# Optimization experiments

Hardware: AMD Instinct MI355X
Metric: run time of the kernel (lower is better)

Reference implementation:

```python
import jax, jax.numpy as jnp
import numpy as np

BETA = 0.1
MARGIN = 0.1
LOSS_WEIGHT = 1.0
K = 4          # num_negative_samples_per_positive
EPS = 1e-6
C, D, P = 100000, 256, 65536


def _energy(p, c):
    """Euclidean entailment-cone energy: relu(apex_angle(p,c) - aperture(p))."""
    diff = c - p
    num = jnp.sum(c * c, -1) - jnp.sum(p * p, -1) - jnp.sum(diff * diff, -1)
    norm_p = jnp.linalg.norm(p, axis=-1)
    denom = 2.0 * norm_p * jnp.linalg.norm(diff, axis=-1) + EPS
    cosang = jnp.clip(num / denom, -1.0 + EPS, 1.0 - EPS)
    ang = jnp.arccos(cosang)
    aperture = jnp.arcsin(jnp.clip(BETA / (norm_p + EPS), 0.0, 1.0 - EPS))
    return jax.nn.relu(ang - aperture)


def setup_inputs() -> dict:
    key = jax.random.key(0)
    k1, k2, k3 = jax.random.split(key, 3)
    prototypes = jax.random.normal(k1, (C, D), dtype=jnp.float32)
    pairs = jax.random.randint(k2, (P, 2), 0, C, dtype=jnp.int32)
    neg_c = jax.random.randint(k3, (P * K,), 0, C, dtype=jnp.int32)
    return {"prototypes": prototypes, "pairs": pairs, "neg_c": neg_c}


def reference(prototypes, pairs, neg_c):
    # positive pairs: (parent, child) gathers
    p_pos = prototypes[pairs[:, 0]]                    # [P, D]
    c_pos = prototypes[pairs[:, 1]]                    # [P, D]
    avg_pos = _energy(p_pos, c_pos).mean()

    # negatives: each positive parent repeated K times vs sampled neg children
    neg_p_idx = jnp.repeat(pairs[:, 0], K)             # [P*K]
    p_neg = prototypes[neg_p_idx]                      # [P*K, D]
    c_neg = prototypes[neg_c]                          # [P*K, D]
    avg_neg = jax.nn.relu(MARGIN - _energy(p_neg, c_neg)).mean()

    return (avg_pos + avg_neg) * 0.5 * LOSS_WEIGHT
```

## Files before the change

kernel.cpp:

```cpp
#include <hip/hip_runtime.h>

#define BETA   0.1f
#define MARGIN 0.1f
#define EPSF   1e-6f
#define KNEG   4

typedef float f2_t __attribute__((ext_vector_type(2)));

__device__ __forceinline__ float gsum16(float v) {
    #pragma unroll
    for (int off = 8; off >= 1; off >>= 1) v += __shfl_xor(v, off, 64);
    return v;
}
__device__ __forceinline__ float wave_sum(float v) {
    #pragma unroll
    for (int off = 32; off >= 1; off >>= 1) v += __shfl_xor(v, off, 64);
    return v;
}
__device__ __forceinline__ float dot4(float4 a, float4 b) {
    return a.x*b.x + a.y*b.y + a.z*b.z + a.w*b.w;
}
__device__ __forceinline__ unsigned packf4(float4 v) {
    unsigned p = __builtin_amdgcn_cvt_pk_fp8_f32(v.x, v.y, 0u, false);
    return __builtin_amdgcn_cvt_pk_fp8_f32(v.z, v.w, p, true);
}
__device__ __forceinline__ void unpack4(unsigned u, float* f) {
    f2_t a = __builtin_amdgcn_cvt_pk_f32_fp8(u, false);
    f[0] = a.x; f[1] = a.y;
    a = __builtin_amdgcn_cvt_pk_f32_fp8(u, true);
    f[2] = a.x; f[3] = a.y;
}

__global__ __launch_bounds__(256) void cvt_fp8_norm(
    const float* __restrict__ in, uint4* __restrict__ tab,
    float* __restrict__ norm2, float* __restrict__ apert, int C)
{
    const int sl  = threadIdx.x & 15;
    const int row = (blockIdx.x * 256 + threadIdx.x) >> 4;
    if (row >= C) return;
    const float4* src = (const float4*)(in + (size_t)row * 256);
    float4 v0 = src[sl], v1 = src[sl + 16], v2 = src[sl + 32], v3 = src[sl + 48];
    uint4 u;
    u.x = packf4(v0); u.y = packf4(v1); u.z = packf4(v2); u.w = packf4(v3);
    tab[(size_t)row * 16 + sl] = u;
    float ss = gsum16(dot4(v0,v0) + dot4(v1,v1) + dot4(v2,v2) + dot4(v3,v3));
    if (sl == 0) {
        norm2[row] = ss;
        float np = sqrtf(ss);
        apert[row] = asinf(fminf(fmaxf(BETA / (np + EPSF), 0.f), 1.f - EPSF));
    }
}

__global__ __launch_bounds__(256) void cone_main_fp8(
    const uint4* __restrict__ tab,
    const float* __restrict__ norm2,
    const float* __restrict__ apert,
    const int*   __restrict__ pairs,
    const int*   __restrict__ negc,
    float*       __restrict__ part,
    int P)
{
    const int lane = threadIdx.x & 63;
    const int wid  = threadIdx.x >> 6;
    const int sub  = lane >> 4;
    const int sl   = lane & 15;
    const int pair = (blockIdx.x * 4 + wid) * 4 + sub;

    float pos_e = 0.f, neg_e = 0.f;
    if (pair < P) {
        const int pi = pairs[2 * pair];
        int idx[5];
        idx[0] = pairs[2 * pair + 1];
        #pragma unroll
        for (int k = 0; k < KNEG; ++k) idx[1 + k] = negc[4 * pair + k];

        uint4 pu = tab[(size_t)pi * 16 + sl];
        uint4 cu[5];
        #pragma unroll
        for (int j = 0; j < 5; ++j) cu[j] = tab[(size_t)idx[j] * 16 + sl];

        int tidx = (sl >= 2 && sl < 7) ? idx[sl - 2] : pi;
        const float* tbl = (sl == 1) ? apert : norm2;
        float sv = tbl[tidx];
        const int base = sub * 16;
        const float p2 = __shfl(sv, base + 0, 64);
        const float ap = __shfl(sv, base + 1, 64);
        const float np = sqrtf(p2);

        float pf[16];
        unpack4(pu.x, pf + 0);  unpack4(pu.y, pf + 4);
        unpack4(pu.z, pf + 8);  unpack4(pu.w, pf + 12);

        #pragma unroll
        for (int j = 0; j < 5; ++j) {
            float cf[16];
            unpack4(cu[j].x, cf + 0);  unpack4(cu[j].y, cf + 4);
            unpack4(cu[j].z, cf + 8);  unpack4(cu[j].w, cf + 12);
            float acc = 0.f;
            #pragma unroll
            for (int d = 0; d < 16; ++d) acc += cf[d] * pf[d];
            float dot = gsum16(acc);
            float c2  = __shfl(sv, base + 2 + j, 64);
            float num = 2.f * (dot - p2);
            float d2  = fmaxf(c2 + p2 - 2.f * dot, 0.f);
            float den = 2.f * np * sqrtf(d2) + EPSF;
            float ca  = fminf(fmaxf(num / den, -1.f + EPSF), 1.f - EPSF);
            float e   = fmaxf(acosf(ca) - ap, 0.f);
            if (j == 0) pos_e = e;
            else        neg_e += fmaxf(MARGIN - e, 0.f);
        }
    }

    __shared__ float sp[16], sn[16];
    if (sl == 0) { sp[wid * 4 + sub] = pos_e; sn[wid * 4 + sub] = neg_e; }
    __syncthreads();
    if (threadIdx.x == 0) {
        float ps = 0.f, ns = 0.f;
        #pragma unroll
        for (int i = 0; i < 16; ++i) { ps += sp[i]; ns += sn[i]; }
        part[2 * blockIdx.x]     = ps;
        part[2 * blockIdx.x + 1] = ns;
    }
}

__global__ __launch_bounds__(256) void cone_main_f32(
    const float* __restrict__ proto,
    const int*   __restrict__ pairs,
    const int*   __restrict__ negc,
    float*       __restrict__ part,
    int P)
{
    const int lane = threadIdx.x & 63;
    const int wid  = threadIdx.x >> 6;
    const int sub  = lane >> 4;
    const int sl   = lane & 15;
    const int pair = (blockIdx.x * 4 + wid) * 4 + sub;

    float pos_e = 0.f, neg_e = 0.f;
    if (pair < P) {
        const int pi = pairs[2 * pair];
        int idx[5];
        idx[0] = pairs[2 * pair + 1];
        #pragma unroll
        for (int k = 0; k < KNEG; ++k) idx[1 + k] = negc[4 * pair + k];

        const float4* prow = (const float4*)(proto + (size_t)pi * 256);
        float4 pv[4];
        #pragma unroll
        for (int r = 0; r < 4; ++r) pv[r] = prow[sl + 16 * r];

        float pp = 0.f;
        #pragma unroll
        for (int r = 0; r < 4; ++r) pp += dot4(pv[r], pv[r]);
        float p2     = gsum16(pp);
        float norm_p = sqrtf(p2);
        float apert  = asinf(fminf(fmaxf(BETA / (norm_p + EPSF), 0.f), 1.f - EPSF));

        #pragma unroll
        for (int j = 0; j < 5; ++j) {
            const float4* crow = (const float4*)(proto + (size_t)idx[j] * 256);
            float cc = 0.f, dd = 0.f;
            #pragma unroll
            for (int r = 0; r < 4; ++r) {
                float4 c = crow[sl + 16 * r], p = pv[r];
                cc += dot4(c, c);
                float dx = c.x - p.x, dy = c.y - p.y, dz = c.z - p.z, dw = c.w - p.w;
                dd += dx*dx + dy*dy + dz*dz + dw*dw;
            }
            float c2 = gsum16(cc);
            float d2 = gsum16(dd);
            float num    = c2 - p2 - d2;
            float den    = 2.f * norm_p * sqrtf(d2) + EPSF;
            float cosang = fminf(fmaxf(num / den, -1.f + EPSF), 1.f - EPSF);
            float e      = fmaxf(acosf(cosang) - apert, 0.f);
            if (j == 0) pos_e = e;
            else        neg_e += fmaxf(MARGIN - e, 0.f);
        }
    }

    __shared__ float sp[16], sn[16];
    if (sl == 0) { sp[wid * 4 + sub] = pos_e; sn[wid * 4 + sub] = neg_e; }
    __syncthreads();
    if (threadIdx.x == 0) {
        float ps = 0.f, ns = 0.f;
        #pragma unroll
        for (int i = 0; i < 16; ++i) { ps += sp[i]; ns += sn[i]; }
        part[2 * blockIdx.x]     = ps;
        part[2 * blockIdx.x + 1] = ns;
    }
}

__global__ __launch_bounds__(1024) void cone_final(
    const float* __restrict__ part, float* __restrict__ out, int nblocks, int P)
{
    float ps = 0.f, ns = 0.f;
    for (int i = threadIdx.x; i < nblocks; i += 1024) {
        ps += part[2 * i];
        ns += part[2 * i + 1];
    }
    ps = wave_sum(ps);
    ns = wave_sum(ns);
    const int lane = threadIdx.x & 63, wid = threadIdx.x >> 6;
    __shared__ float sp[16], sn[16];
    if (lane == 0) { sp[wid] = ps; sn[wid] = ns; }
    __syncthreads();
    if (threadIdx.x == 0) {
        float tp = 0.f, tn = 0.f;
        #pragma unroll
        for (int i = 0; i < 16; ++i) { tp += sp[i]; tn += sn[i]; }
        float fP = (float)P;
        out[0] = (tp / fP + tn / (fP * (float)KNEG)) * 0.5f;
    }
}

extern "C" void kernel_launch(void* const* d_in, const int* in_sizes, int n_in,
                              void* d_out, int out_size, void* d_ws, size_t ws_size,
                              hipStream_t stream) {
    const float* proto = (const float*)d_in[0];
    const int*   pairs = (const int*)d_in[1];
    const int*   negc  = (const int*)d_in[2];
    const int P = in_sizes[1] / 2;
    const int C = in_sizes[0] / 256;
    const int nblocks = (P + 15) / 16;

    const size_t tab_bytes = (size_t)in_sizes[0];
    const size_t need = tab_bytes + (size_t)C * 2 * sizeof(float)
                      + (size_t)nblocks * 2 * sizeof(float);

    if (ws_size >= need) {
        uint4* tab   = (uint4*)d_ws;
        float* norm2 = (float*)((char*)d_ws + tab_bytes);
        float* apert = norm2 + C;
        float* part  = apert + C;
        cvt_fp8_norm<<<(C + 15) / 16, 256, 0, stream>>>(proto, tab, norm2, apert, C);
        cone_main_fp8<<<nblocks, 256, 0, stream>>>(tab, norm2, apert, pairs, negc, part, P);
        cone_final<<<1, 1024, 0, stream>>>(part, (float*)d_out, nblocks, P);
    } else {
        float* part = (float*)d_ws;
        cone_main_f32<<<nblocks, 256, 0, stream>>>(proto, pairs, negc, part, P);
        cone_final<<<1, 1024, 0, stream>>>(part, (float*)d_out, nblocks, P);
    }
}
```

Baseline: 174.7 us.

## Quantize prototype table to per-row int4 and fuse final reduction via last-block counter

Replaces the per-call fp8 copy of the prototype table with a 4-bit symmetric per-row quantization. Each row gets a scale, stored with the squared norm and aperture in one float4 side record, so every gather reads 128 bytes plus one 16-byte record instead of 256 bytes plus separate norm and aperture loads. The dot product is rebuilt from the raw codes using a zero-point correction and the two row scales. The separate final-reduction kernel is dropped in favour of an atomic counter, so the last block sums the partials, at the cost of a memset launch. Int4 is much coarser than fp8, so the parent-child dot product (and through it the angle) may lose accuracy, while the norms stay exact.

```diff
diff --git a/kernel.cpp b/kernel.cpp
--- a/kernel.cpp
+++ b/kernel.cpp
@@ -5,13 +5,16 @@
 #define EPSF   1e-6f
 #define KNEG   4
 
-typedef float f2_t __attribute__((ext_vector_type(2)));
-
 __device__ __forceinline__ float gsum16(float v) {
     #pragma unroll
     for (int off = 8; off >= 1; off >>= 1) v += __shfl_xor(v, off, 64);
     return v;
 }
+__device__ __forceinline__ float gmax16(float v) {
+    #pragma unroll
+    for (int off = 8; off >= 1; off >>= 1) v = fmaxf(v, __shfl_xor(v, off, 64));
+    return v;
+}
 __device__ __forceinline__ float wave_sum(float v) {
     #pragma unroll
     for (int off = 32; off >= 1; off >>= 1) v += __shfl_xor(v, off, 64);
@@ -20,45 +23,54 @@
 __device__ __forceinline__ float dot4(float4 a, float4 b) {
     return a.x*b.x + a.y*b.y + a.z*b.z + a.w*b.w;
 }
-__device__ __forceinline__ unsigned packf4(float4 v) {
-    unsigned p = __builtin_amdgcn_cvt_pk_fp8_f32(v.x, v.y, 0u, false);
-    return __builtin_amdgcn_cvt_pk_fp8_f32(v.z, v.w, p, true);
-}
-__device__ __forceinline__ void unpack4(unsigned u, float* f) {
-    f2_t a = __builtin_amdgcn_cvt_pk_f32_fp8(u, false);
-    f[0] = a.x; f[1] = a.y;
-    a = __builtin_amdgcn_cvt_pk_f32_fp8(u, true);
-    f[2] = a.x; f[3] = a.y;
-}
-
-__global__ __launch_bounds__(256) void cvt_fp8_norm(
-    const float* __restrict__ in, uint4* __restrict__ tab,
-    float* __restrict__ norm2, float* __restrict__ apert, int C)
+
+__global__ __launch_bounds__(256) void cvt_i4(
+    const float* __restrict__ in, uint2* __restrict__ tab,
+    float4* __restrict__ side, int C)
 {
     const int sl  = threadIdx.x & 15;
     const int row = (blockIdx.x * 256 + threadIdx.x) >> 4;
     if (row >= C) return;
     const float4* src = (const float4*)(in + (size_t)row * 256);
-    float4 v0 = src[sl], v1 = src[sl + 16], v2 = src[sl + 32], v3 = src[sl + 48];
-    uint4 u;
-    u.x = packf4(v0); u.y = packf4(v1); u.z = packf4(v2); u.w = packf4(v3);
-    tab[(size_t)row * 16 + sl] = u;
+    float4 v0 = src[4*sl+0], v1 = src[4*sl+1], v2 = src[4*sl+2], v3 = src[4*sl+3];
+    float f[16] = { v0.x, v0.y, v0.z, v0.w,  v1.x, v1.y, v1.z, v1.w,
+                    v2.x, v2.y, v2.z, v2.w,  v3.x, v3.y, v3.z, v3.w };
+    float am = 0.f;
+    #pragma unroll
+    for (int d = 0; d < 16; ++d) am = fmaxf(am, fabsf(f[d]));
+    am = gmax16(am);
+    const float inv = (am > 0.f) ? (7.5f / am) : 0.f;
+    unsigned u0 = 0, u1 = 0;
+    #pragma unroll
+    for (int n = 0; n < 8; ++n) {
+        int c = (int)rintf(f[n] * inv);
+        c = (c < -8) ? -8 : ((c > 7) ? 7 : c);
+        u0 |= (unsigned)(c + 8) << (4 * n);
+    }
+    #pragma unroll
+    for (int n = 0; n < 8; ++n) {
+        int c = (int)rintf(f[8 + n] * inv);
+        c = (c < -8) ? -8 : ((c > 7) ? 7 : c);
+        u1 |= (unsigned)(c + 8) << (4 * n);
+    }
+    tab[(size_t)row * 16 + sl] = make_uint2(u0, u1);
     float ss = gsum16(dot4(v0,v0) + dot4(v1,v1) + dot4(v2,v2) + dot4(v3,v3));
     if (sl == 0) {
-        norm2[row] = ss;
         float np = sqrtf(ss);
-        apert[row] = asinf(fminf(fmaxf(BETA / (np + EPSF), 0.f), 1.f - EPSF));
-    }
-}
-
-__global__ __launch_bounds__(256) void cone_main_fp8(
-    const uint4* __restrict__ tab,
-    const float* __restrict__ norm2,
-    const float* __restrict__ apert,
-    const int*   __restrict__ pairs,
-    const int*   __restrict__ negc,
-    float*       __restrict__ part,
-    int P)
+        float ap = asinf(fminf(fmaxf(BETA / (np + EPSF), 0.f), 1.f - EPSF));
+        side[row] = make_float4(ss, ap, am * (1.f / 7.5f), 0.f);
+    }
+}
+
+__global__ __launch_bounds__(256) void cone_main_i4(
+    const uint2*  __restrict__ tab,
+    const float4* __restrict__ side,
+    const int*    __restrict__ pairs,
+    const int*    __restrict__ negc,
+    float*        __restrict__ part,
+    unsigned*     __restrict__ counter,
+    float*        __restrict__ out,
+    int P, int nblocks)
 {
     const int lane = threadIdx.x & 63;
     const int wid  = threadIdx.x >> 6;
@@ -74,52 +86,83 @@
         #pragma unroll
         for (int k = 0; k < KNEG; ++k) idx[1 + k] = negc[4 * pair + k];
 
-        uint4 pu = tab[(size_t)pi * 16 + sl];
-        uint4 cu[5];
+        uint2 pu = tab[(size_t)pi * 16 + sl];
+        uint2 cu[5];
         #pragma unroll
         for (int j = 0; j < 5; ++j) cu[j] = tab[(size_t)idx[j] * 16 + sl];
 
-        int tidx = (sl >= 2 && sl < 7) ? idx[sl - 2] : pi;
-        const float* tbl = (sl == 1) ? apert : norm2;
-        float sv = tbl[tidx];
+        int tidx = (sl >= 1 && sl < 6) ? idx[sl - 1] : pi;
+        float4 sd = side[tidx];
         const int base = sub * 16;
-        const float p2 = __shfl(sv, base + 0, 64);
-        const float ap = __shfl(sv, base + 1, 64);
-        const float np = sqrtf(p2);
+        const float p2  = __shfl(sd.x, base + 0, 64);
+        const float ap  = __shfl(sd.y, base + 0, 64);
+        const float sp  = __shfl(sd.z, base + 0, 64);
+        const float np  = sqrtf(p2);
 
         float pf[16];
-        unpack4(pu.x, pf + 0);  unpack4(pu.y, pf + 4);
-        unpack4(pu.z, pf + 8);  unpack4(pu.w, pf + 12);
+        #pragma unroll
+        for (int n = 0; n < 8; ++n) pf[n]     = (float)((pu.x >> (4*n)) & 0xF) - 8.f;
+        #pragma unroll
+        for (int n = 0; n < 8; ++n) pf[8 + n] = (float)((pu.y >> (4*n)) & 0xF) - 8.f;
+        float s = 0.f;
+        #pragma unroll
+        for (int d = 0; d < 16; ++d) s += pf[d];
+        const float SP = gsum16(s);
 
         #pragma unroll
         for (int j = 0; j < 5; ++j) {
-            float cf[16];
-            unpack4(cu[j].x, cf + 0);  unpack4(cu[j].y, cf + 4);
-            unpack4(cu[j].z, cf + 8);  unpack4(cu[j].w, cf + 12);
             float acc = 0.f;
             #pragma unroll
-            for (int d = 0; d < 16; ++d) acc += cf[d] * pf[d];
-            float dot = gsum16(acc);
-            float c2  = __shfl(sv, base + 2 + j, 64);
-            float num = 2.f * (dot - p2);
-            float d2  = fmaxf(c2 + p2 - 2.f * dot, 0.f);
-            float den = 2.f * np * sqrtf(d2) + EPSF;
-            float ca  = fminf(fmaxf(num / den, -1.f + EPSF), 1.f - EPSF);
-            float e   = fmaxf(acosf(ca) - ap, 0.f);
+            for (int n = 0; n < 8; ++n)
+                acc = fmaf((float)((cu[j].x >> (4*n)) & 0xF), pf[n], acc);
+            #pragma unroll
+            for (int n = 0; n < 8; ++n)
+                acc = fmaf((float)((cu[j].y >> (4*n)) & 0xF), pf[8 + n], acc);
+            const float draw = gsum16(acc) - 8.f * SP;
+            const float c2 = __shfl(sd.x, base + 1 + j, 64);
+            const float sc = __shfl(sd.z, base + 1 + j, 64);
+            const float dot = draw * sp * sc;
+            const float num = 2.f * (dot - p2);
+            const float d2  = fmaxf(c2 + p2 - 2.f * dot, 0.f);
+            const float den = 2.f * np * sqrtf(d2) + EPSF;
+            const float ca  = fminf(fmaxf(num / den, -1.f + EPSF), 1.f - EPSF);
+            const float e   = fmaxf(acosf(ca) - ap, 0.f);
             if (j == 0) pos_e = e;
             else        neg_e += fmaxf(MARGIN - e, 0.f);
         }
     }
 
-    __shared__ float sp[16], sn[16];
-    if (sl == 0) { sp[wid * 4 + sub] = pos_e; sn[wid * 4 + sub] = neg_e; }
+    __shared__ float spos[16], sneg[16];
+    __shared__ int   isLast;
+    if (sl == 0) { spos[wid * 4 + sub] = pos_e; sneg[wid * 4 + sub] = neg_e; }
     __syncthreads();
     if (threadIdx.x == 0) {
         float ps = 0.f, ns = 0.f;
         #pragma unroll
-        for (int i = 0; i < 16; ++i) { ps += sp[i]; ns += sn[i]; }
+        for (int i = 0; i < 16; ++i) { ps += spos[i]; ns += sneg[i]; }
         part[2 * blockIdx.x]     = ps;
         part[2 * blockIdx.x + 1] = ns;
+        __threadfence();
+        unsigned t = atomicAdd(counter, 1u);
+        isLast = (t == (unsigned)(nblocks - 1));
+    }
+    __syncthreads();
+    if (isLast) {
+        float ps = 0.f, ns = 0.f;
+        for (int i = threadIdx.x; i < nblocks; i += 256) {
+            ps += part[2 * i];
+            ns += part[2 * i + 1];
+        }
+        ps = wave_sum(ps);
+        ns = wave_sum(ns);
+        if (sl == 0) { spos[wid] = ps; sneg[wid] = ns; }
+        __syncthreads();
+        if (threadIdx.x == 0) {
+            float tp = spos[0] + spos[1] + spos[2] + spos[3];
+            float tn = sneg[0] + sneg[1] + sneg[2] + sneg[3];
+            float fP = (float)P;
+            out[0] = (tp / fP + tn / (fP * (float)KNEG)) * 0.5f;
+        }
     }
 }
 
@@ -223,18 +266,22 @@
     const int C = in_sizes[0] / 256;
     const int nblocks = (P + 15) / 16;
 
-    const size_t tab_bytes = (size_t)in_sizes[0];
-    const size_t need = tab_bytes + (size_t)C * 2 * sizeof(float)
-                      + (size_t)nblocks * 2 * sizeof(float);
+    const size_t tab_bytes  = (size_t)C * 128;
+    const size_t side_bytes = (size_t)C * 16;
+    const size_t part_bytes = (size_t)nblocks * 2 * sizeof(float);
+    const size_t need = tab_bytes + side_bytes + part_bytes + 256;
 
     if (ws_size >= need) {
-        uint4* tab   = (uint4*)d_ws;
-        float* norm2 = (float*)((char*)d_ws + tab_bytes);
-        float* apert = norm2 + C;
-        float* part  = apert + C;
-        cvt_fp8_norm<<<(C + 15) / 16, 256, 0, stream>>>(proto, tab, norm2, apert, C);
-        cone_main_fp8<<<nblocks, 256, 0, stream>>>(tab, norm2, apert, pairs, negc, part, P);
-        cone_final<<<1, 1024, 0, stream>>>(part, (float*)d_out, nblocks, P);
+        char* base = (char*)d_ws;
+        uint2*    tab     = (uint2*)base;
+        float4*   side    = (float4*)(base + tab_bytes);
+        float*    part    = (float*)(base + tab_bytes + side_bytes);
+        unsigned* counter = (unsigned*)(base + tab_bytes + side_bytes + part_bytes);
+
+        hipMemsetAsync(counter, 0, sizeof(unsigned), stream);
+        cvt_i4<<<(C + 15) / 16, 256, 0, stream>>>(proto, tab, side, C);
+        cone_main_i4<<<nblocks, 256, 0, stream>>>(tab, side, pairs, negc, part,
+                                                  counter, (float*)d_out, P, nblocks);
     } else {
         float* part = (float*)d_ws;
         cone_main_f32<<<nblocks, 256, 0, stream>>>(proto, pairs, negc, part, P);
```

Result: slower. 274.5 us (+57.1%).
